# Kernel optimization log

Measured on AMD Instinct MI355X. Metric: run time of the kernel, lower is better.

Reference implementation:

```python
import jax, jax.numpy as jnp
import numpy as np

HF, WF = 361, 720            # full-res equiangular grid (0.5 deg)
HP, WP = 90, 180             # processor grid (scale_factor=4)
CIN, CE, COUT = 26, 48, 24   # input chans, embed dim (4*8+8+8), output chans
K, NB = 9, 6                 # DISCO kernel basis count (3x3 morlet), nnz per output pixel
L = M = 90                   # SHT lmax / mmax on processor grid
NL = 4                       # processor blocks (even: SFNO global, odd: local DISCO)


def _make_psi(Ho, Wo, Hi, Wi, rng):
    # sparse quadrature-weighted DISCO basis: for each output pixel, NB neighbor
    # columns into the (Hi,Wi) input grid and K basis values per nonzero.
    lat = np.round(np.arange(Ho) * (Hi - 1) / max(Ho - 1, 1)).astype(np.int64)
    lon = np.round(np.arange(Wo) * Wi / Wo).astype(np.int64)
    LAT, LON = np.meshgrid(lat, lon, indexing='ij')
    offs = [(0, 0), (0, 1), (0, -1), (1, 0), (-1, 0), (1, 1)][:NB]
    idx = np.stack([np.clip(LAT + dy, 0, Hi - 1) * Wi + (LON + dx) % Wi for dy, dx in offs], -1)
    idx = idx.reshape(Ho * Wo, NB)
    vals = rng.standard_normal((K, Ho * Wo, NB)).astype(np.float32)
    vals /= np.abs(vals).sum(-1, keepdims=True) + 1e-6   # 'mean' basis normalization
    return jnp.asarray(idx, jnp.int32), jnp.asarray(vals)


def _make_leg(rng):
    # Legendre-transform matrices (quadrature-weighted fwd, inverse), m<=l triangular
    mask = (np.arange(M)[None, :] <= np.arange(L)[:, None]).astype(np.float32)
    Pw = rng.standard_normal((L, M, HP)).astype(np.float32) * mask[:, :, None] / np.sqrt(HP)
    Pi = rng.standard_normal((L, M, HP)).astype(np.float32) * mask[:, :, None] / np.sqrt(L)
    return jnp.asarray(Pw), jnp.asarray(Pi)


def _interp1d(n_out, n_in, periodic):
    if periodic:
        src = np.arange(n_out) * n_in / n_out
        i0 = np.floor(src).astype(np.int64) % n_in
        i1 = (i0 + 1) % n_in
    else:
        src = np.arange(n_out) * (n_in - 1) / (n_out - 1)
        i0 = np.floor(src).astype(np.int64)
        i1 = np.minimum(i0 + 1, n_in - 1)
    w = (src - np.floor(src)).astype(np.float32)
    return jnp.asarray(i0, jnp.int32), jnp.asarray(i1, jnp.int32), jnp.asarray(w)


def disco_conv(x, idx, vals, w):
    # x [B,Ci,Pin], idx [Pout,NB] int32, vals [K,Pout,NB], w [Co,Ci,K]
    xg = x[:, :, idx]                                   # [B,Ci,Pout,NB] sparse gather
    z = jnp.einsum('kpn,bipn->bikp', vals, xg)          # [B,Ci,K,Pout]
    return jnp.einsum('oik,bikp->bop', w, z)            # [B,Co,Pout]


def sht(g, Pw):
    xf = jnp.fft.rfft(g, axis=-1)[..., :M] / WP         # [B,C,HP,M] complex
    return jnp.einsum('lmt,bctm->bclm', Pw, xf)         # [B,C,L,M]


def isht(c, Pi):
    xf = jnp.einsum('lmt,bclm->bctm', Pi, c)            # [B,C,HP,M]
    full = jnp.zeros(xf.shape[:-1] + (WP // 2 + 1,), xf.dtype).at[..., :M].set(xf)
    return jnp.fft.irfft(full * WP, n=WP, axis=-1)


def _fwd(x, enc_psi_vals, enc_w, proc_psi_vals, lw, gw, Pw, Pi, m1, m2, ls,
         lat_w, lon_w, dec_psi_vals, dec_w,
         enc_psi_idx, proc_psi_idx, dec_psi_idx, lat_i0, lat_i1, lon_i0, lon_i1):
    B = x.shape[0]
    # encoder: full-res -> processor-grid DISCO conv (fp32 block in original)
    h = disco_conv(x.reshape(B, CIN, HF * WF), enc_psi_idx, enc_psi_vals, enc_w)
    for i in range(NL):
        if i % 2 == 0:  # SFNO global block: SHT -> per-degree dhconv -> ISHT
            c = sht(h.reshape(B, CE, HP, WP), Pw)
            c = jnp.einsum('oil,bilm->bolm', gw[i // 2], c)
            dx = isht(c, Pi).reshape(B, CE, HP * WP)
        else:           # local DISCO block
            dx = disco_conv(h, proc_psi_idx, proc_psi_vals, lw[i // 2])
        # norm = identity ('none'); MLP (1x1 convs) + GELU; layer_scale; identity skip
        dx = jax.nn.gelu(jnp.einsum('hi,bip->bhp', m1[i], dx))
        dx = jnp.einsum('oh,bhp->bop', m2[i], dx)
        h = h + ls[i][None, :, None] * dx
    # decoder: bilinear resample to full res, then full-res DISCO conv
    g = h.reshape(B, CE, HP, WP)
    u = g[:, :, lat_i0, :] * (1.0 - lat_w)[None, None, :, None] \
        + g[:, :, lat_i1, :] * lat_w[None, None, :, None]
    u = u[:, :, :, lon_i0] * (1.0 - lon_w) + u[:, :, :, lon_i1] * lon_w
    y = disco_conv(u.reshape(B, CE, HF * WF), dec_psi_idx, dec_psi_vals, dec_w)
    return y.reshape(B, COUT, HF, WF)


def setup_inputs() -> dict:
    rng = np.random.default_rng(0)
    key = jax.random.key(0)
    sn = lambda *s: jnp.asarray(rng.standard_normal(s).astype(np.float32))
    x = jax.random.normal(key, (1, CIN, HF, WF), jnp.float32)
    enc_psi_idx, enc_psi_vals = _make_psi(HP, WP, HF, WF, rng)
    proc_psi_idx, proc_psi_vals = _make_psi(HP, WP, HP, WP, rng)
    dec_psi_idx, dec_psi_vals = _make_psi(HF, WF, HF, WF, rng)
    Pw, Pi = _make_leg(rng)
    lat_i0, lat_i1, lat_w = _interp1d(HF, HP, False)
    lon_i0, lon_i1, lon_w = _interp1d(WF, WP, True)
    HD = int(2.0 * CE)
    return {
        'x': x,
        'enc_psi_idx': enc_psi_idx, 'enc_psi_vals': enc_psi_vals,
        'enc_w': 0.1 * sn(CE, CIN, K),
        'proc_psi_idx': proc_psi_idx, 'proc_psi_vals': proc_psi_vals,
        'lw': 0.1 * sn(2, CE, CE, K), 'gw': 0.1 * sn(2, CE, CE, L),
        'Pw': Pw, 'Pi': Pi,
        'm1': sn(NL, HD, CE) / np.float32(np.sqrt(CE)),
        'm2': sn(NL, CE, HD) / np.float32(np.sqrt(HD)),
        'ls': 0.1 * jnp.ones((NL, CE), jnp.float32),
        'lat_i0': lat_i0, 'lat_i1': lat_i1, 'lat_w': lat_w,
        'lon_i0': lon_i0, 'lon_i1': lon_i1, 'lon_w': lon_w,
        'dec_psi_idx': dec_psi_idx, 'dec_psi_vals': dec_psi_vals,
        'dec_w': 0.1 * sn(COUT, CE, K),
    }


def reference(x, enc_psi_idx, enc_psi_vals, enc_w, proc_psi_idx, proc_psi_vals, lw, gw,
              Pw, Pi, m1, m2, ls, lat_i0, lat_i1, lat_w, lon_i0, lon_i1, lon_w,
              dec_psi_idx, dec_psi_vals, dec_w):
    return _fwd(x, enc_psi_vals, enc_w, proc_psi_vals, lw, gw, Pw, Pi, m1, m2, ls,
                lat_w, lon_w, dec_psi_vals, dec_w,
                enc_psi_idx, proc_psi_idx, dec_psi_idx, lat_i0, lat_i1, lon_i0, lon_i1)
```

## Files before the change

### kernel.cpp

```cpp
#include <hip/hip_runtime.h>
#include <math.h>

constexpr int kHF = 361, kWF = 720;
constexpr int kHP = 90,  kWP = 180;
constexpr int kCIN = 26, kCE = 48, kCOUT = 24;
constexpr int kK = 9, kNB = 6;
constexpr int kL = 90, kM = 90;
constexpr int kNL = 4, kHD = 96;
constexpr int kNP  = kHP * kWP;
constexpr int kNPF = kHF * kWF;

#ifndef M_PI
#define M_PI 3.14159265358979323846
#endif

__global__ __launch_bounds__(256) void k_prep1(float2* __restrict__ fcs, float2* __restrict__ icn,
                                               const float* __restrict__ dw, float* __restrict__ dwT) {
    int t = blockIdx.x * 256 + threadIdx.x;
    if (t < kM * kWP) {
        int m = t / kWP, w = t % kWP;
        double th = (2.0 * M_PI / (double)kWP) * (double)(m * w);
        double c = cos(th), s = sin(th);
        fcs[w * kM + m] = make_float2((float)(c / (double)kWP), (float)(-s / (double)kWP));
        float sc = (m == 0) ? 1.0f : 2.0f;
        icn[m * kWP + w] = make_float2(sc * (float)c, sc * (float)s);
    }
    if (t < kCOUT * kCE * kK) {
        int k = t % kK;
        int i = (t / kK) % kCE;
        int o = t / (kK * kCE);
        dwT[((size_t)i * kCOUT + o) * kK + k] = dw[t];
    }
}

__global__ __launch_bounds__(256) void k_prep2(const float* __restrict__ Pw, const float* __restrict__ Pi,
                                               float* __restrict__ PwT, float* __restrict__ PiT) {
    int t = blockIdx.x * 256 + threadIdx.x;
    int N = kL * kM * kHP;
    if (t >= 2 * N) return;
    int mode = t >= N ? 1 : 0;
    int u = mode ? t - N : t;
    int l = u / (kM * kHP);
    int r = u % (kM * kHP);
    int m = r / kHP;
    int tt = r % kHP;
    if (mode == 0) PwT[(l * kHP + tt) * kM + m] = Pw[u];
    else           PiT[(tt * kL + l) * kM + m] = Pi[u];
}

template <int TCIN, int TCOUT, int OG>
__global__ __launch_bounds__(256) void k_disco(const float* __restrict__ src, int srcStride,
                                               const int* __restrict__ idx, const float* __restrict__ vals,
                                               const float* __restrict__ w, float* __restrict__ out, int np) {
    int gt = blockIdx.x * 256 + threadIdx.x;
    if (gt >= np * OG) return;
    int p = gt % np;
    int og = gt / np;
    constexpr int OC = TCOUT / OG;

    int qi[kNB];
#pragma unroll
    for (int n = 0; n < kNB; n++) qi[n] = idx[p * kNB + n];

    float vv[kK][kNB];
#pragma unroll
    for (int k = 0; k < kK; k++) {
        const float* vp = vals + ((size_t)k * np + p) * kNB;
#pragma unroll
        for (int n = 0; n < kNB; n += 2) {
            float2 v2 = *(const float2*)(vp + n);
            vv[k][n] = v2.x; vv[k][n + 1] = v2.y;
        }
    }

    float acc[OC];
#pragma unroll
    for (int o = 0; o < OC; o++) acc[o] = 0.0f;

    const float* wbase = w + (size_t)og * OC * TCIN * kK;

    for (int i = 0; i < TCIN; i++) {
        float xg[kNB];
#pragma unroll
        for (int n = 0; n < kNB; n++) xg[n] = src[i * srcStride + qi[n]];
        float z[kK];
#pragma unroll
        for (int k = 0; k < kK; k++) {
            float zz = 0.0f;
#pragma unroll
            for (int n = 0; n < kNB; n++) zz = fmaf(vv[k][n], xg[n], zz);
            z[k] = zz;
        }
#pragma unroll
        for (int o = 0; o < OC; o++) {
            const float* wp = wbase + ((size_t)o * TCIN + i) * kK;
            float s = acc[o];
#pragma unroll
            for (int k = 0; k < kK; k++) s = fmaf(wp[k], z[k], s);
            acc[o] = s;
        }
    }
#pragma unroll
    for (int o = 0; o < OC; o++) out[(size_t)(og * OC + o) * np + p] = acc[o];
}

__global__ __launch_bounds__(256) void k_rfft3(const float* __restrict__ g, const float2* __restrict__ fcs,
                                               float2* __restrict__ xc) {
    __shared__ float gs[8 * kWP];
    int t0 = blockIdx.x * 256;
    int t = t0 + threadIdx.x;
    constexpr int NPAIR = (kCE * kHP) / 2;
    int rp0 = t0 / kM;
    int rp1 = (t0 + 255) / kM;
    int r0 = 2 * rp0;
    int nrows = 2 * (rp1 - rp0 + 1);
    for (int j = threadIdx.x; j < nrows * kWP; j += 256) {
        int rr = j / kWP, w = j % kWP;
        int row = r0 + rr;
        if (row < kCE * kHP) gs[j] = g[(size_t)row * kWP + w];
    }
    __syncthreads();
    if (t >= NPAIR * kM) return;
    int m = t % kM;
    int rp = t / kM;
    const float* g0 = &gs[(2 * rp - r0) * kWP];
    const float* g1 = g0 + kWP;
    float ar0 = 0.0f, ai0 = 0.0f, ar1 = 0.0f, ai1 = 0.0f;
#pragma unroll 6
    for (int w = 0; w < kWP; w++) {
        float2 f = fcs[w * kM + m];
        float a = g0[w], b = g1[w];
        ar0 = fmaf(a, f.x, ar0); ai0 = fmaf(a, f.y, ai0);
        ar1 = fmaf(b, f.x, ar1); ai1 = fmaf(b, f.y, ai1);
    }
    xc[(size_t)(2 * rp) * kM + m]     = make_float2(ar0, ai0);
    xc[(size_t)(2 * rp + 1) * kM + m] = make_float2(ar1, ai1);
}

constexpr int kMT = 18;
__global__ __launch_bounds__(256) void k_sht_gmix2(const float* __restrict__ PwT,
                                                   const float2* __restrict__ xc,
                                                   const float* __restrict__ gwl,
                                                   float2* __restrict__ c2c) {
    __shared__ float2 cs[kCE][kMT];
    int l = blockIdx.x / 5;
    int m0 = (blockIdx.x % 5) * kMT;
    int tid = threadIdx.x;

    if (tid < 12 * kMT) {
        int ig = tid / kMT, mm = tid % kMT;
        int i = ig * 4;
        int m = m0 + mm;
        float ar0 = 0, ai0 = 0, ar1 = 0, ai1 = 0, ar2 = 0, ai2 = 0, ar3 = 0, ai3 = 0;
        const float*  pw = PwT + (size_t)l * kHP * kM + m;
        const float2* x0 = xc + (size_t)(i + 0) * kHP * kM + m;
        const float2* x1 = xc + (size_t)(i + 1) * kHP * kM + m;
        const float2* x2 = xc + (size_t)(i + 2) * kHP * kM + m;
        const float2* x3 = xc + (size_t)(i + 3) * kHP * kM + m;
#pragma unroll 3
        for (int tt = 0; tt < kHP; tt++) {
            float pv = pw[tt * kM];
            float2 a = x0[tt * kM], b = x1[tt * kM], c = x2[tt * kM], d = x3[tt * kM];
            ar0 = fmaf(pv, a.x, ar0); ai0 = fmaf(pv, a.y, ai0);
            ar1 = fmaf(pv, b.x, ar1); ai1 = fmaf(pv, b.y, ai1);
            ar2 = fmaf(pv, c.x, ar2); ai2 = fmaf(pv, c.y, ai2);
            ar3 = fmaf(pv, d.x, ar3); ai3 = fmaf(pv, d.y, ai3);
        }
        cs[i + 0][mm] = make_float2(ar0, ai0);
        cs[i + 1][mm] = make_float2(ar1, ai1);
        cs[i + 2][mm] = make_float2(ar2, ai2);
        cs[i + 3][mm] = make_float2(ar3, ai3);
    }
    __syncthreads();
    for (int j = tid; j < kCE * kMT; j += 256) {
        int o = j / kMT, mm = j % kMT;
        float ar = 0.0f, ai = 0.0f;
        const float* gv = gwl + (size_t)o * kCE * kL + l;
#pragma unroll 8
        for (int i = 0; i < kCE; i++) {
            float g = gv[(size_t)i * kL];
            float2 cv = cs[i][mm];
            ar = fmaf(g, cv.x, ar);
            ai = fmaf(g, cv.y, ai);
        }
        c2c[((size_t)o * kL + l) * kM + m0 + mm] = make_float2(ar, ai);
    }
}

constexpr int kCG = 4;
__global__ __launch_bounds__(192) void k_isht_irfft2(const float* __restrict__ PiT,
                                                     const float2* __restrict__ c2c,
                                                     const float2* __restrict__ icn,
                                                     float* __restrict__ dx) {
    __shared__ float2 xm[kCG][kM];
    int bi = blockIdx.x;
    int t = bi % kHP;
    int c0 = (bi / kHP) * kCG;
    int tid = threadIdx.x;

    if (tid < 2 * kM) {
        int m = tid % kM;
        int cp = tid / kM;
        int ca = c0 + cp * 2;
        float ar0 = 0, ai0 = 0, ar1 = 0, ai1 = 0;
        const float*  pv  = PiT + (size_t)t * kL * kM + m;
        const float2* cva = c2c + (size_t)ca * kL * kM + m;
        const float2* cvb = cva + (size_t)kL * kM;
#pragma unroll 6
        for (int l = 0; l < kL; l++) {
            float pp = pv[(size_t)l * kM];
            float2 a = cva[(size_t)l * kM];
            float2 b = cvb[(size_t)l * kM];
            ar0 = fmaf(pp, a.x, ar0); ai0 = fmaf(pp, a.y, ai0);
            ar1 = fmaf(pp, b.x, ar1); ai1 = fmaf(pp, b.y, ai1);
        }
        xm[cp * 2 + 0][m] = make_float2(ar0, ai0);
        xm[cp * 2 + 1][m] = make_float2(ar1, ai1);
    }
    __syncthreads();
    if (tid < kWP) {
        int w = tid;
        float a0 = 0, a1 = 0, a2 = 0, a3 = 0;
#pragma unroll 6
        for (int m = 0; m < kM; m++) {
            float2 f = icn[m * kWP + w];
            float2 x0 = xm[0][m], x1 = xm[1][m], x2 = xm[2][m], x3 = xm[3][m];
            a0 = fmaf(x0.x, f.x, a0); a0 = fmaf(-x0.y, f.y, a0);
            a1 = fmaf(x1.x, f.x, a1); a1 = fmaf(-x1.y, f.y, a1);
            a2 = fmaf(x2.x, f.x, a2); a2 = fmaf(-x2.y, f.y, a2);
            a3 = fmaf(x3.x, f.x, a3); a3 = fmaf(-x3.y, f.y, a3);
        }
        dx[((size_t)(c0 + 0) * kHP + t) * kWP + w] = a0;
        dx[((size_t)(c0 + 1) * kHP + t) * kWP + w] = a1;
        dx[((size_t)(c0 + 2) * kHP + t) * kWP + w] = a2;
        dx[((size_t)(c0 + 3) * kHP + t) * kWP + w] = a3;
    }
}

__device__ __forceinline__ float gelu_tanh(float x) {
    float x3 = x * x * x;
    float t = tanhf(0.7978845608028654f * (x + 0.044715f * x3));
    return 0.5f * x * (1.0f + t);
}

constexpr int kTP = 32;
__global__ __launch_bounds__(256) void k_mlp_f(const float* __restrict__ m1w, const float* __restrict__ m2w,
                                               const float* __restrict__ lsw, const float* __restrict__ dx,
                                               float* __restrict__ h) {
    __shared__ float xs[kCE][kTP];
    __shared__ float g1[kHD][kTP];
    int p0 = blockIdx.x * kTP;
    int tid = threadIdx.x;

    for (int j = tid; j < kCE * kTP; j += 256) {
        int i = j / kTP, pp = j % kTP;
        int p = p0 + pp;
        xs[i][pp] = (p < kNP) ? dx[(size_t)i * kNP + p] : 0.0f;
    }
    __syncthreads();
    for (int j = tid; j < kHD * kTP; j += 256) {
        int hh = j / kTP, pp = j % kTP;
        const float* w1 = m1w + (size_t)hh * kCE;
        float a = 0.0f;
#pragma unroll 8
        for (int i = 0; i < kCE; i++) a = fmaf(w1[i], xs[i][pp], a);
        g1[hh][pp] = gelu_tanh(a);
    }
    __syncthreads();
    for (int j = tid; j < kCE * kTP; j += 256) {
        int o = j / kTP, pp = j % kTP;
        int p = p0 + pp;
        if (p < kNP) {
            const float* w2 = m2w + (size_t)o * kHD;
            float a = 0.0f;
#pragma unroll 8
            for (int jj = 0; jj < kHD; jj++) a = fmaf(w2[jj], g1[jj][pp], a);
            size_t q = (size_t)o * kNP + p;
            h[q] = h[q] + lsw[o] * a;
        }
    }
}

__global__ __launch_bounds__(256) void k_dconv_d(const float* __restrict__ h,
                                                 const float* __restrict__ dvals,
                                                 const float* __restrict__ dwT,
                                                 const int* __restrict__ li0, const int* __restrict__ li1,
                                                 const float* __restrict__ lwt, const int* __restrict__ oi0,
                                                 const int* __restrict__ oi1, const float* __restrict__ owt,
                                                 float* __restrict__ out) {
    int p = blockIdx.x * 256 + threadIdx.x;
    if (p >= kNPF) return;
    int lat = p / kWF;
    int p_lon = p - lat * kWF;

    int i0r[3], i1r[3];
    float awr[3];
#pragma unroll
    for (int r = 0; r < 3; r++) {
        int Lr = lat - 1 + r;
        Lr = Lr < 0 ? 0 : (Lr > kHF - 1 ? kHF - 1 : Lr);
        i0r[r] = li0[Lr]; i1r[r] = li1[Lr]; awr[r] = lwt[Lr];
    }
    int F = min(i0r[0], min(i0r[1], i0r[2]));

    float wrow[3][3];
#pragma unroll
    for (int r = 0; r < 3; r++) {
        int r0 = i0r[r] - F, r1 = i1r[r] - F;
#pragma unroll
        for (int pr = 0; pr < 3; pr++) {
            float wv = 0.0f;
            if (pr == r0) wv += 1.0f - awr[r];
            if (pr == r1) wv += awr[r];
            wrow[r][pr] = wv;
        }
    }

    int o0d[3], o1d[3];
    float owd[3];
#pragma unroll
    for (int d = 0; d < 3; d++) {
        int lm = (p_lon + d - 1 + kWF) % kWF;
        o0d[d] = oi0[lm]; o1d[d] = oi1[lm]; owd[d] = owt[lm];
    }
    int G = o0d[0];
    float wcol[3][3];
#pragma unroll
    for (int d = 0; d < 3; d++) {
        int c0 = (o0d[d] - G + kWP) % kWP;
        int c1 = (o1d[d] - G + kWP) % kWP;
#pragma unroll
        for (int pc = 0; pc < 3; pc++) {
            float wv = 0.0f;
            if (pc == c0) wv += 1.0f - owd[d];
            if (pc == c1) wv += owd[d];
            wcol[d][pc] = wv;
        }
    }

    float vv[kK][kNB];
#pragma unroll
    for (int k = 0; k < kK; k++) {
        const float* vp = dvals + ((size_t)k * kNPF + p) * kNB;
#pragma unroll
        for (int n = 0; n < kNB; n += 2) {
            float2 v2 = *(const float2*)(vp + n);
            vv[k][n] = v2.x; vv[k][n + 1] = v2.y;
        }
    }

    const int RR[kNB] = {1, 1, 1, 2, 0, 2};
    const int CC[kNB] = {1, 2, 0, 1, 1, 2};
    float ck[kK][3][3];
#pragma unroll
    for (int k = 0; k < kK; k++)
#pragma unroll
        for (int pr = 0; pr < 3; pr++)
#pragma unroll
            for (int pc = 0; pc < 3; pc++) {
                float s = 0.0f;
#pragma unroll
                for (int n = 0; n < kNB; n++)
                    s = fmaf(vv[k][n], wrow[RR[n]][pr] * wcol[CC[n]][pc], s);
                ck[k][pr][pc] = s;
            }

    int ofs[3][3];
#pragma unroll
    for (int pr = 0; pr < 3; pr++) {
        int row = F + pr; row = row > kHP - 1 ? kHP - 1 : row;
#pragma unroll
        for (int pc = 0; pc < 3; pc++) {
            int col = (G + pc) % kWP;
            ofs[pr][pc] = row * kWP + col;
        }
    }

    float acc[kCOUT];
#pragma unroll
    for (int o = 0; o < kCOUT; o++) acc[o] = 0.0f;

    const float* wp = dwT;
    const float* hi = h;
#pragma unroll 2
    for (int i = 0; i < kCE; i++) {
        float hv[3][3];
#pragma unroll
        for (int pr = 0; pr < 3; pr++)
#pragma unroll
            for (int pc = 0; pc < 3; pc++)
                hv[pr][pc] = hi[ofs[pr][pc]];
        float z[kK];
#pragma unroll
        for (int k = 0; k < kK; k++) {
            float s = 0.0f;
#pragma unroll
            for (int pr = 0; pr < 3; pr++)
#pragma unroll
                for (int pc = 0; pc < 3; pc++)
                    s = fmaf(ck[k][pr][pc], hv[pr][pc], s);
            z[k] = s;
        }
#pragma unroll
        for (int o = 0; o < kCOUT; o++) {
            float s = acc[o];
#pragma unroll
            for (int k = 0; k < kK; k++) s = fmaf(wp[o * kK + k], z[k], s);
            acc[o] = s;
        }
        wp += kCOUT * kK;
        hi += kNP;
    }

#pragma unroll
    for (int o = 0; o < kCOUT; o++) out[(size_t)o * kNPF + p] = acc[o];
}

extern "C" void kernel_launch(void* const* d_in, const int* in_sizes, int n_in,
                              void* d_out, int out_size, void* d_ws, size_t ws_size,
                              hipStream_t stream) {
    const float* x         = (const float*)d_in[0];
    const int*   enc_idx   = (const int*)d_in[1];
    const float* enc_vals  = (const float*)d_in[2];
    const float* enc_w     = (const float*)d_in[3];
    const int*   proc_idx  = (const int*)d_in[4];
    const float* proc_vals = (const float*)d_in[5];
    const float* lw        = (const float*)d_in[6];
    const float* gw        = (const float*)d_in[7];
    const float* Pw        = (const float*)d_in[8];
    const float* Pi        = (const float*)d_in[9];
    const float* m1        = (const float*)d_in[10];
    const float* m2        = (const float*)d_in[11];
    const float* ls        = (const float*)d_in[12];
    const int*   li0       = (const int*)d_in[13];
    const int*   li1       = (const int*)d_in[14];
    const float* lwt       = (const float*)d_in[15];
    const int*   oi0       = (const int*)d_in[16];
    const int*   oi1       = (const int*)d_in[17];
    const float* owt       = (const float*)d_in[18];
    const int*   dec_idx   = (const int*)d_in[19];
    const float* dec_vals  = (const float*)d_in[20];
    const float* dec_w     = (const float*)d_in[21];
    float* out = (float*)d_out;
    (void)dec_idx;

    float* ws = (float*)d_ws;
    size_t off = 0;
    auto alloc = [&](size_t n) { float* p = ws + off; off += n; return p; };
    float*  h    = alloc((size_t)kCE * kNP);
    float2* xc   = (float2*)alloc((size_t)2 * kCE * kHP * kM);
    float2* c2c  = (float2*)alloc((size_t)2 * kCE * kL * kM);
    float*  dx   = alloc((size_t)kCE * kNP);
    float2* fcs  = (float2*)alloc((size_t)2 * kM * kWP);
    float2* icn  = (float2*)alloc((size_t)2 * kM * kWP);
    float*  PwT  = alloc((size_t)kL * kM * kHP);
    float*  PiT  = alloc((size_t)kL * kM * kHP);
    float*  dwT  = alloc((size_t)kCOUT * kCE * kK);
    (void)ws_size; (void)in_sizes; (void)n_in; (void)out_size;

    dim3 B(256);
    auto nb = [](long long n) { return dim3((unsigned)((n + 255) / 256)); };

    k_prep1<<<nb(kM * kWP), B, 0, stream>>>(fcs, icn, dec_w, dwT);
    k_prep2<<<nb(2LL * kL * kM * kHP), B, 0, stream>>>(Pw, Pi, PwT, PiT);

    k_disco<kCIN, kCE, 8><<<nb((long long)kNP * 8), B, 0, stream>>>(
        x, kNPF, enc_idx, enc_vals, enc_w, h, kNP);

    int nMlpBlocks = (kNP + kTP - 1) / kTP;
    for (int i = 0; i < kNL; i++) {
        if (i % 2 == 0) {
            const float* gwl = gw + (size_t)(i / 2) * kCE * kCE * kL;
            k_rfft3<<<nb((long long)(kCE * kHP / 2) * kM), B, 0, stream>>>(h, fcs, xc);
            k_sht_gmix2<<<dim3(kL * 5), B, 0, stream>>>(PwT, xc, gwl, c2c);
            k_isht_irfft2<<<dim3(kHP * (kCE / kCG)), dim3(192), 0, stream>>>(PiT, c2c, icn, dx);
        } else {
            const float* lwl = lw + (size_t)(i / 2) * kCE * kCE * kK;
            k_disco<kCE, kCE, 8><<<nb((long long)kNP * 8), B, 0, stream>>>(
                h, kNP, proc_idx, proc_vals, lwl, dx, kNP);
        }
        k_mlp_f<<<dim3(nMlpBlocks), B, 0, stream>>>(
            m1 + (size_t)i * kHD * kCE, m2 + (size_t)i * kCE * kHD, ls + (size_t)i * kCE, dx, h);
    }

    k_dconv_d<<<nb((long long)kNPF), B, 0, stream>>>(h, dec_vals, dwT,
                                                     li0, li1, lwt, oi0, oi1, owt, out);
}
```

Before: 713.3 us.

## Split decoder output channels across threads, raise DISCO groups, merge prep kernels

The decoder DISCO kernel now divides its 24 output channels into two groups handled by separate threads. This doubles the thread count and halves per-thread accumulators, at the cost of recomputing the interpolation and basis setup in both groups. The encoder and processor DISCO kernels use 16 output groups instead of 8, the MLP pixel tile shrinks from 32 to 16 to launch more blocks, and the two prep kernels are merged into one launch. The extra parallelism is meant to improve occupancy and latency hiding on the large full-resolution decoder, in exchange for redundant work and more reloads of the input.

```diff
diff --git a/kernel.cpp b/kernel.cpp
--- a/kernel.cpp
+++ b/kernel.cpp
@@ -14,8 +14,10 @@
 #define M_PI 3.14159265358979323846
 #endif
 
-__global__ __launch_bounds__(256) void k_prep1(float2* __restrict__ fcs, float2* __restrict__ icn,
-                                               const float* __restrict__ dw, float* __restrict__ dwT) {
+__global__ __launch_bounds__(256) void k_prep(float2* __restrict__ fcs, float2* __restrict__ icn,
+                                              const float* __restrict__ dw, float* __restrict__ dwT,
+                                              const float* __restrict__ Pw, const float* __restrict__ Pi,
+                                              float* __restrict__ PwT, float* __restrict__ PiT) {
     int t = blockIdx.x * 256 + threadIdx.x;
     if (t < kM * kWP) {
         int m = t / kWP, w = t % kWP;
@@ -31,21 +33,17 @@
         int o = t / (kK * kCE);
         dwT[((size_t)i * kCOUT + o) * kK + k] = dw[t];
     }
-}
-
-__global__ __launch_bounds__(256) void k_prep2(const float* __restrict__ Pw, const float* __restrict__ Pi,
-                                               float* __restrict__ PwT, float* __restrict__ PiT) {
-    int t = blockIdx.x * 256 + threadIdx.x;
     int N = kL * kM * kHP;
-    if (t >= 2 * N) return;
-    int mode = t >= N ? 1 : 0;
-    int u = mode ? t - N : t;
-    int l = u / (kM * kHP);
-    int r = u % (kM * kHP);
-    int m = r / kHP;
-    int tt = r % kHP;
-    if (mode == 0) PwT[(l * kHP + tt) * kM + m] = Pw[u];
-    else           PiT[(tt * kL + l) * kM + m] = Pi[u];
+    if (t < 2 * N) {
+        int mode = t >= N ? 1 : 0;
+        int u = mode ? t - N : t;
+        int l = u / (kM * kHP);
+        int r = u % (kM * kHP);
+        int m = r / kHP;
+        int tt = r % kHP;
+        if (mode == 0) PwT[(l * kHP + tt) * kM + m] = Pw[u];
+        else           PiT[(tt * kL + l) * kM + m] = Pi[u];
+    }
 }
 
 template <int TCIN, int TCOUT, int OG>
@@ -243,7 +241,7 @@
     return 0.5f * x * (1.0f + t);
 }
 
-constexpr int kTP = 32;
+constexpr int kTP = 16;
 __global__ __launch_bounds__(256) void k_mlp_f(const float* __restrict__ m1w, const float* __restrict__ m2w,
                                                const float* __restrict__ lsw, const float* __restrict__ dx,
                                                float* __restrict__ h) {
@@ -281,15 +279,18 @@
     }
 }
 
-__global__ __launch_bounds__(256) void k_dconv_d(const float* __restrict__ h,
-                                                 const float* __restrict__ dvals,
-                                                 const float* __restrict__ dwT,
-                                                 const int* __restrict__ li0, const int* __restrict__ li1,
-                                                 const float* __restrict__ lwt, const int* __restrict__ oi0,
-                                                 const int* __restrict__ oi1, const float* __restrict__ owt,
-                                                 float* __restrict__ out) {
-    int p = blockIdx.x * 256 + threadIdx.x;
-    if (p >= kNPF) return;
+__global__ __launch_bounds__(256) void k_dconv_o2(const float* __restrict__ h,
+                                                  const float* __restrict__ dvals,
+                                                  const float* __restrict__ dwT,
+                                                  const int* __restrict__ li0, const int* __restrict__ li1,
+                                                  const float* __restrict__ lwt, const int* __restrict__ oi0,
+                                                  const int* __restrict__ oi1, const float* __restrict__ owt,
+                                                  float* __restrict__ out) {
+    constexpr int OG = 2, OC = kCOUT / OG;
+    int gt = blockIdx.x * 256 + threadIdx.x;
+    if (gt >= kNPF * OG) return;
+    int p = gt % kNPF;
+    int og = gt / kNPF;
     int lat = p / kWF;
     int p_lon = p - lat * kWF;
 
@@ -376,11 +377,11 @@
         }
     }
 
-    float acc[kCOUT];
-#pragma unroll
-    for (int o = 0; o < kCOUT; o++) acc[o] = 0.0f;
-
-    const float* wp = dwT;
+    float acc[OC];
+#pragma unroll
+    for (int o = 0; o < OC; o++) acc[o] = 0.0f;
+
+    const float* wp = dwT + (size_t)og * OC * kK;
     const float* hi = h;
 #pragma unroll 2
     for (int i = 0; i < kCE; i++) {
@@ -402,7 +403,7 @@
             z[k] = s;
         }
 #pragma unroll
-        for (int o = 0; o < kCOUT; o++) {
+        for (int o = 0; o < OC; o++) {
             float s = acc[o];
 #pragma unroll
             for (int k = 0; k < kK; k++) s = fmaf(wp[o * kK + k], z[k], s);
@@ -413,7 +414,7 @@
     }
 
 #pragma unroll
-    for (int o = 0; o < kCOUT; o++) out[(size_t)o * kNPF + p] = acc[o];
+    for (int o = 0; o < OC; o++) out[(size_t)(og * OC + o) * kNPF + p] = acc[o];
 }
 
 extern "C" void kernel_launch(void* const* d_in, const int* in_sizes, int n_in,
@@ -461,10 +462,9 @@
     dim3 B(256);
     auto nb = [](long long n) { return dim3((unsigned)((n + 255) / 256)); };
 
-    k_prep1<<<nb(kM * kWP), B, 0, stream>>>(fcs, icn, dec_w, dwT);
-    k_prep2<<<nb(2LL * kL * kM * kHP), B, 0, stream>>>(Pw, Pi, PwT, PiT);
-
-    k_disco<kCIN, kCE, 8><<<nb((long long)kNP * 8), B, 0, stream>>>(
+    k_prep<<<nb(2LL * kL * kM * kHP), B, 0, stream>>>(fcs, icn, dec_w, dwT, Pw, Pi, PwT, PiT);
+
+    k_disco<kCIN, kCE, 16><<<nb((long long)kNP * 16), B, 0, stream>>>(
         x, kNPF, enc_idx, enc_vals, enc_w, h, kNP);
 
     int nMlpBlocks = (kNP + kTP - 1) / kTP;
@@ -476,13 +476,13 @@
             k_isht_irfft2<<<dim3(kHP * (kCE / kCG)), dim3(192), 0, stream>>>(PiT, c2c, icn, dx);
         } else {
             const float* lwl = lw + (size_t)(i / 2) * kCE * kCE * kK;
-            k_disco<kCE, kCE, 8><<<nb((long long)kNP * 8), B, 0, stream>>>(
+            k_disco<kCE, kCE, 16><<<nb((long long)kNP * 16), B, 0, stream>>>(
                 h, kNP, proc_idx, proc_vals, lwl, dx, kNP);
         }
         k_mlp_f<<<dim3(nMlpBlocks), B, 0, stream>>>(
             m1 + (size_t)i * kHD * kCE, m2 + (size_t)i * kCE * kHD, ls + (size_t)i * kCE, dx, h);
     }
 
-    k_dconv_d<<<nb((long long)kNPF), B, 0, stream>>>(h, dec_vals, dwT,
-                                                     li0, li1, lwt, oi0, oi1, owt, out);
-}
+    k_dconv_o2<<<nb((long long)kNPF * 2), B, 0, stream>>>(h, dec_vals, dwT,
+                                                          li0, li1, lwt, oi0, oi1, owt, out);
+}
```

Measured after the change: 972.1 us. 36.3% more time.
